# Performance work log

Hardware: AMD Instinct MI355X
Metric: run time of the kernel (lower is better)

Reference implementation:

```python
import jax, jax.numpy as jnp
import numpy as np

B, T, S, D, H, F = 4, 1024, 1024, 1024, 16, 4096
NEG = jnp.float32(-1e9)


def _ln(x, g, b):
    m = jnp.mean(x, axis=-1, keepdims=True)
    v = jnp.mean((x - m) ** 2, axis=-1, keepdims=True)
    return (x - m) * jax.lax.rsqrt(v + 1e-5) * g + b


def _mha(q, k, v, wq, bq, wk, bk, wv, bv, wo, bo, scale, mask, causal, sbias):
    Bq, Tq, Dq = q.shape
    Sk = k.shape[1]
    dk = Dq // H
    Q = (q @ wq.T + bq).reshape(Bq, Tq, H, dk).transpose(0, 2, 1, 3)  # [B,H,T,dk]
    K = (k @ wk.T + bk).reshape(Bq, Sk, H, dk).transpose(0, 2, 1, 3)  # [B,H,S,dk]
    V = (v @ wv.T + bv).reshape(Bq, Sk, H, dk).transpose(0, 2, 1, 3)
    s = jnp.einsum('bhtd,bhsd->bhts', Q, K) / jnp.sqrt(jnp.float32(dk))
    if sbias is not None:
        s = s + scale * sbias[:, None, None, :]
    if mask is not None:
        s = jnp.where(mask == 0, NEG, s)
    if causal is not None:
        s = jnp.where(causal == 0, NEG, s)
    a = jax.nn.softmax(s, axis=-1)
    o = jnp.einsum('bhts,bhsd->bhtd', a, V).transpose(0, 2, 1, 3).reshape(Bq, Tq, Dq)
    return o @ wo.T + bo


def setup_inputs():
    key = jax.random.key(0)
    ks = jax.random.split(key, 16)
    r = lambda i, shape, s=0.02: jax.random.normal(ks[i], shape, dtype=jnp.float32) * s
    z = lambda *shape: jnp.zeros(shape, jnp.float32)
    o = lambda *shape: jnp.ones(shape, jnp.float32)
    inp = dict(
        x=r(0, (B, T, D), 1.0),
        memory=r(1, (B, S, D), 1.0),
        sentence_bias=r(2, (B, S), 1.0),
        trg_mask=jnp.ones((B, 1, 1, T), jnp.int32),
        trg_causal_mask=jnp.tril(jnp.ones((T, T), jnp.int32))[None, None],
        src_mask=jnp.ones((B, 1, 1, S), jnp.int32),
        sa_wq=r(3, (D, D)), sa_bq=z(D), sa_wk=r(4, (D, D)), sa_bk=z(D),
        sa_wv=r(5, (D, D)), sa_bv=z(D), sa_wo=r(6, (D, D)), sa_bo=z(D),
        sa_scale=jnp.float32(0.1),
        ca_wq=r(7, (D, D)), ca_bq=z(D), ca_wk=r(8, (D, D)), ca_bk=z(D),
        ca_wv=r(9, (D, D)), ca_bv=z(D), ca_wo=r(10, (D, D)), ca_bo=z(D),
        ca_scale=jnp.float32(0.1),
        ln1_g=o(D), ln1_b=z(D), ln2_g=o(D), ln2_b=z(D), ln3_g=o(D), ln3_b=z(D),
        ffn_w1=r(11, (F, D)), ffn_b1=z(F), ffn_w2=r(12, (D, F)), ffn_b2=z(D),
    )
    return inp


def reference(x, memory, trg_mask, trg_causal_mask, src_mask, sentence_bias,
              sa_wq, sa_bq, sa_wk, sa_bk, sa_wv, sa_bv, sa_wo, sa_bo, sa_scale,
              ca_wq, ca_bq, ca_wk, ca_bk, ca_wv, ca_bv, ca_wo, ca_bo, ca_scale,
              ln1_g, ln1_b, ln2_g, ln2_b, ln3_g, ln3_b,
              ffn_w1, ffn_b1, ffn_w2, ffn_b2):
    # Faithful quirk: Q comes from normed x, K/V from raw residual stream.
    x = x + _mha(_ln(x, ln1_g, ln1_b), x, x,
                 sa_wq, sa_bq, sa_wk, sa_bk, sa_wv, sa_bv, sa_wo, sa_bo,
                 sa_scale, trg_mask, trg_causal_mask, None)
    x = x + _mha(_ln(x, ln2_g, ln2_b), memory, memory,
                 ca_wq, ca_bq, ca_wk, ca_bk, ca_wv, ca_bv, ca_wo, ca_bo,
                 ca_scale, src_mask, None, sentence_bias)
    h = _ln(x, ln3_g, ln3_b)
    x = x + (jax.nn.relu(h @ ffn_w1.T + ffn_b1) @ ffn_w2.T + ffn_b2)
    return x
```

## Files before the change

kernel.cpp:

```cpp
#include <hip/hip_runtime.h>
#include <hip/hip_bf16.h>
#include <cmath>
#include <stdint.h>

typedef __hip_bfloat16 bf16;
typedef __attribute__((ext_vector_type(8))) __bf16 bf16x8;
typedef __attribute__((ext_vector_type(8))) unsigned short u16x8;
typedef __attribute__((ext_vector_type(4))) float f32x4;

__device__ __forceinline__ void gld16(const void* g, const void* l)
{
    __builtin_amdgcn_global_load_lds(
        (const __attribute__((address_space(1))) unsigned int*)(unsigned long long)g,
        (__attribute__((address_space(3))) unsigned int*)(unsigned int)(unsigned long long)l,
        16, 0, 0);
}

struct CvtSrcs { const float* p[24]; };

__global__ __launch_bounds__(256) void cvt_all(CvtSrcs s, bf16* __restrict__ dst)
{
    const int i = (blockIdx.x * 256 + threadIdx.x) * 8;
    const int seg = i >> 20;
    const float* sp = s.p[seg] + (i & 1048575);
    const float4 a = *(const float4*)(sp);
    const float4 b = *(const float4*)(sp + 4);
    const float v[8] = {a.x, a.y, a.z, a.w, b.x, b.y, b.z, b.w};
    bf16 tmp[8];
#pragma unroll
    for (int j = 0; j < 8; ++j) tmp[j] = __float2bfloat16(v[j]);
    *(uint4*)(dst + i) = *(const uint4*)tmp;
}

enum {
    EPI_QSCALE = 0,
    EPI_KV = 1,
    EPI_RELU = 2,
    EPI_RES_F32_F32OUT = 3,
    EPI_PART = 4
};

template <int EPI>
__global__ __launch_bounds__(512, 2) void gemm256(
    const bf16* __restrict__ A, const bf16* __restrict__ W,
    const float* __restrict__ bias, void* __restrict__ out,
    int N, int Kiter, int Kstride)
{
    __shared__ __align__(16) unsigned short sA[2][2][128 * 64];
    __shared__ __align__(16) unsigned short sB[2][2][128 * 64];

    const int t  = threadIdx.x;
    const int l  = t & 63;
    const int w  = t >> 6;
    const int wv = w * 64;
    const int wr = w >> 2;
    const int wc = w & 3;
    const int lm = l & 15;
    const int kq = l >> 4;
    const int rx = lm & 7;

    int bx = blockIdx.x;
    if (EPI == EPI_PART) {
        const int chunk = bx >> 6;
        bx &= 63;
        A += (size_t)chunk * 1024;
        W += (size_t)chunk * 1024;
        out = (void*)((bf16*)out + (size_t)chunk * 4096 * 1024);
    }
    const int xcd = bx & 7;
    const int ib  = bx >> 3;
    const int bm  = xcd * 2 + (ib & 1);
    const int bn  = ib >> 1;

    const bf16* gA = A + (size_t)(bm * 256 + (t >> 3)) * Kstride
                       + ((t & 7) ^ ((t >> 3) & 7)) * 8;
    const bf16* gB = W + (size_t)(bn * 256 + (t >> 3)) * Kstride
                       + ((t & 7) ^ ((t >> 3) & 7)) * 8;

#define STAGE(slot, kt)                                                       \
    do {                                                                      \
        _Pragma("unroll")                                                     \
        for (int h = 0; h < 2; ++h) {                                         \
            _Pragma("unroll")                                                 \
            for (int j = 0; j < 2; ++j) {                                     \
                gld16(gA + (size_t)(h * 128 + j * 64) * Kstride + (kt) * 64,  \
                      &sA[slot][h][(j * 512 + wv) * 8]);                      \
                gld16(gB + (size_t)(h * 128 + j * 64) * Kstride + (kt) * 64,  \
                      &sB[slot][h][(j * 512 + wv) * 8]);                      \
            }                                                                 \
        }                                                                     \
    } while (0)

    STAGE(0, 0);
    __syncthreads();

    f32x4 acc[8][4] = {};
    const int NT = Kiter >> 6;

    for (int tt = 0; tt < NT; ++tt) {
        const int s = tt & 1;
        if (tt + 1 < NT) STAGE(s ^ 1, tt + 1);

#pragma unroll
        for (int q = 0; q < 4; ++q) {
            const int mh = q >> 1, nh = q & 1;
            bf16x8 af[4][2], bg[2][2];
#pragma unroll
            for (int mi = 0; mi < 4; ++mi)
#pragma unroll
                for (int kk = 0; kk < 2; ++kk) {
                    const int lr = mh * 64 + mi * 16 + lm;
                    const int sl = ((kk << 2) | kq) ^ rx;
                    af[mi][kk] = __builtin_bit_cast(bf16x8,
                        *(const u16x8*)(&sA[s][wr][lr * 64 + sl * 8]));
                }
#pragma unroll
            for (int ni = 0; ni < 2; ++ni)
#pragma unroll
                for (int kk = 0; kk < 2; ++kk) {
                    const int lr = (wc & 1) * 64 + nh * 32 + ni * 16 + lm;
                    const int sl = ((kk << 2) | kq) ^ rx;
                    bg[ni][kk] = __builtin_bit_cast(bf16x8,
                        *(const u16x8*)(&sB[s][wc >> 1][lr * 64 + sl * 8]));
                }
            __builtin_amdgcn_s_setprio(1);
#pragma unroll
            for (int mi = 0; mi < 4; ++mi)
#pragma unroll
                for (int ni = 0; ni < 2; ++ni)
#pragma unroll
                    for (int kk = 0; kk < 2; ++kk)
                        acc[mh * 4 + mi][nh * 2 + ni] =
                            __builtin_amdgcn_mfma_f32_16x16x32_bf16(
                                af[mi][kk], bg[ni][kk],
                                acc[mh * 4 + mi][nh * 2 + ni], 0, 0, 0);
            __builtin_amdgcn_s_setprio(0);
        }
        __syncthreads();
    }
#undef STAGE

#pragma unroll
    for (int NI = 0; NI < 4; ++NI) {
        const int col = bn * 256 + wc * 64 + NI * 16 + lm;
        const float bv = (EPI == EPI_PART) ? 0.f : bias[col];
#pragma unroll
        for (int MI = 0; MI < 8; ++MI) {
            const int row = bm * 256 + wr * 128 + MI * 16 + kq * 4;
#pragma unroll
            for (int r = 0; r < 4; ++r) {
                float v = acc[MI][NI][r] + bv;
                if (EPI == EPI_RELU) v = fmaxf(v, 0.f);
                ((bf16*)out)[(size_t)(row + r) * N + col] = __float2bfloat16(v);
            }
        }
    }
}

template <int EPI, int BM>
__global__ __launch_bounds__(BM * 2, 2) void gemm_bt(
    const bf16* __restrict__ A, const bf16* __restrict__ W,
    const float* __restrict__ bias, const float* __restrict__ bias2,
    const float* __restrict__ res, void* __restrict__ out,
    int M, int N, int Kiter, int Kstride)
{
    constexpr int T    = BM * 2;
    constexpr int ISSA = (BM * 4) / T;
    constexpr int ISSB = 512 / T;
    constexpr int ROWS = T / 4;
    constexpr int MBK  = 4096 / BM;
    constexpr int MBX  = MBK / 8;
    constexpr int MBS  = (BM == 64) ? 3 : 2;

    __shared__ __align__(16) unsigned short sA[2][BM * 32];
    __shared__ __align__(16) unsigned short sB[2][128 * 32];

    const int t  = threadIdx.x;
    const int l  = t & 63;
    const int w  = t >> 6;
    const int wv = w * 64;
    const int wm = (w >> 1) * 64;
    const int wn = (w & 1) * 64;
    const int lm = l & 15;
    const int kq = l >> 4;

    int bx = blockIdx.x;
    const int xcd = bx & 7;
    const int ib  = bx >> 3;
    const int bm  = xcd * MBX + (ib & (MBX - 1));
    const int bn  = ib >> MBS;

    const bf16* gA = A + (size_t)(bm * BM + (t >> 2)) * Kstride + (t & 3) * 8;
    const bf16* gB = W + (size_t)(bn * 128 + (t >> 2)) * Kstride + (t & 3) * 8;

    int aoffs[4], boffs[4];
#pragma unroll
    for (int i = 0; i < 4; ++i) {
        aoffs[i] = (wm + i * 16 + lm) * 32 + kq * 8;
        boffs[i] = (wn + i * 16 + lm) * 32 + kq * 8;
    }

#define STAGE(buf, kk)                                                       \
    do {                                                                     \
        _Pragma("unroll")                                                    \
        for (int j = 0; j < ISSA; ++j)                                       \
            gld16(gA + (size_t)j * ROWS * Kstride + (kk),                    \
                  &sA[buf][(j * T + wv) * 8]);                               \
        _Pragma("unroll")                                                    \
        for (int j = 0; j < ISSB; ++j)                                       \
            gld16(gB + (size_t)j * ROWS * Kstride + (kk),                    \
                  &sB[buf][(j * T + wv) * 8]);                               \
    } while (0)

    STAGE(0, 0);
    __syncthreads();

    f32x4 acc[4][4] = {};

    for (int k0 = 0; k0 < Kiter; k0 += 32) {
        const int cur = (k0 >> 5) & 1;

        if (k0 + 32 < Kiter) STAGE(cur ^ 1, k0 + 32);

        bf16x8 af[4], bg[4];
#pragma unroll
        for (int i = 0; i < 4; ++i)
            af[i] = __builtin_bit_cast(bf16x8, *(const u16x8*)(&sA[cur][aoffs[i]]));
#pragma unroll
        for (int i = 0; i < 4; ++i)
            bg[i] = __builtin_bit_cast(bf16x8, *(const u16x8*)(&sB[cur][boffs[i]]));
#pragma unroll
        for (int mi = 0; mi < 4; ++mi)
#pragma unroll
            for (int ni = 0; ni < 4; ++ni)
                acc[mi][ni] = __builtin_amdgcn_mfma_f32_16x16x32_bf16(
                    af[mi], bg[ni], acc[mi][ni], 0, 0, 0);

        __syncthreads();
    }
#undef STAGE

#pragma unroll
    for (int ni = 0; ni < 4; ++ni) {
        const int col = bn * 128 + wn + ni * 16 + lm;
        float bv = 0.f;
        if (EPI == EPI_KV) bv = (col < 1024) ? bias[col] : bias2[col - 1024];
        else bv = bias[col];
#pragma unroll
        for (int mi = 0; mi < 4; ++mi) {
#pragma unroll
            for (int r = 0; r < 4; ++r) {
                const int row = bm * BM + wm + mi * 16 + kq * 4 + r;
                float v = acc[mi][ni][r] + bv;
                if (EPI == EPI_QSCALE) v *= 0.125f;
                if (EPI == EPI_KV) {
                    if (col < 1024) {
                        ((bf16*)out)[(size_t)row * 1024 + col] = __float2bfloat16(v);
                    } else {
                        const int ch = col - 1024;
                        const size_t idx = (size_t)4 * 1048576 +
                            ((size_t)((row >> 10) * 16 + (ch >> 6)) * 64 + (ch & 63)) * 1024
                            + (row & 1023);
                        ((bf16*)out)[idx] = __float2bfloat16(v);
                    }
                } else if (EPI == EPI_RES_F32_F32OUT) {
                    const size_t idx = (size_t)row * N + col;
                    ((float*)out)[idx] = v + res[idx];
                } else {
                    ((bf16*)out)[(size_t)row * N + col] = __float2bfloat16(v);
                }
            }
        }
    }
}

__global__ __launch_bounds__(256) void ffn2_reduce(
    const bf16* __restrict__ P, const float* __restrict__ x2,
    const float* __restrict__ b2, float* __restrict__ out)
{
    const int i = (blockIdx.x * 256 + threadIdx.x) * 8;
    float v[8];
    {
        const float4 a = *(const float4*)(x2 + i);
        const float4 b = *(const float4*)(x2 + i + 4);
        v[0]=a.x; v[1]=a.y; v[2]=a.z; v[3]=a.w; v[4]=b.x; v[5]=b.y; v[6]=b.z; v[7]=b.w;
    }
    const int cb = i & 1023;
#pragma unroll
    for (int j = 0; j < 8; ++j) v[j] += b2[cb + j];
#pragma unroll
    for (int c = 0; c < 4; ++c) {
        const u16x8 u = *(const u16x8*)(P + (size_t)c * 4194304 + i);
        const bf16x8 pb = __builtin_bit_cast(bf16x8, u);
#pragma unroll
        for (int j = 0; j < 8; ++j) v[j] += (float)pb[j];
    }
    float4 o0 = {v[0], v[1], v[2], v[3]}, o1 = {v[4], v[5], v[6], v[7]};
    *(float4*)(out + i) = o0;
    *(float4*)(out + i + 4) = o1;
}

template <bool CAUSAL, bool SBIAS>
__global__ __launch_bounds__(256, 2) void flash_attn(
    const bf16* __restrict__ Q, const bf16* __restrict__ K,
    const bf16* __restrict__ Vt, bf16* __restrict__ O,
    const float* __restrict__ sbias, const float* __restrict__ scale_ptr)
{
    __shared__ __align__(16) unsigned short sK[2][64 * 64];
    __shared__ __align__(16) unsigned short sV[2][64 * 64];
    __shared__ __align__(16) unsigned short sP[4 * 32 * 72];

    const int t  = threadIdx.x;
    const int l  = t & 63;
    const int w  = t >> 6;
    const int wv = w * 64;
    const int lm = l & 15;
    const int kq = l >> 4;

    const int qb = blockIdx.x & 7;
    const int bh = blockIdx.x >> 3;
    const int h  = bh & 15;
    const int b  = bh >> 4;

    const int tb = qb * 128 + w * 32;
    const size_t qrow0 = (size_t)(b * 1024 + tb) * 1024 + h * 64;

    bf16x8 qf[2][2];
#pragma unroll
    for (int mi = 0; mi < 2; ++mi)
#pragma unroll
        for (int kk = 0; kk < 2; ++kk)
            qf[mi][kk] = __builtin_bit_cast(bf16x8,
                *(const u16x8*)(Q + qrow0 + (size_t)(mi * 16 + lm) * 1024 + kk * 32 + kq * 8));

    float cs = 0.f; const float* sb = nullptr;
    if (SBIAS) { cs = scale_ptr[0]; sb = sbias + b * 1024; }

    const bf16* gK = K  + (size_t)(b * 1024 + (t >> 2)) * 1024 + h * 64 + (t & 3) * 8;
    const bf16* gV = Vt + (size_t)((b * 16 + h) * 64 + (t >> 2)) * 1024 + (t & 3) * 8;
    __bf16* sPw = (__bf16*)sP + w * 32 * 72;

#define STAGE_KV(buf, s0r)                                              \
    do {                                                                \
        gld16(gK + (size_t)(s0r) * 1024,      &sK[buf][wv * 8]);        \
        gld16(gK + (size_t)(s0r) * 1024 + 32, &sK[buf][wv * 8 + 2048]); \
        gld16(gV + (s0r),                     &sV[buf][wv * 8]);        \
        gld16(gV + (s0r) + 32,                &sV[buf][wv * 8 + 2048]); \
    } while (0)

    const int niter = CAUSAL ? (2 * qb + 2) : 16;

    STAGE_KV(0, 0);
    __syncthreads();

    f32x4 acc_o[2][4] = {};
    f32x4 l_run[2] = {};

    for (int it = 0; it < niter; ++it) {
        const int s0 = it * 64;
        const int cur = it & 1;

        if (it + 1 < niter) STAGE_KV(cur ^ 1, s0 + 64);

        f32x4 accs[2][4] = {};
#pragma unroll
        for (int ni = 0; ni < 4; ++ni)
#pragma unroll
            for (int kk = 0; kk < 2; ++kk) {
                const bf16x8 kf = __builtin_bit_cast(bf16x8,
                    *(const u16x8*)(&sK[cur][kk * 2048 + (ni * 16 + lm) * 32 + kq * 8]));
#pragma unroll
                for (int mi = 0; mi < 2; ++mi)
                    accs[mi][ni] = __builtin_amdgcn_mfma_f32_16x16x32_bf16(
                        qf[mi][kk], kf, accs[mi][ni], 0, 0, 0);
            }

        if (SBIAS) {
#pragma unroll
            for (int ni = 0; ni < 4; ++ni) {
                const float sv = cs * sb[s0 + ni * 16 + lm];
#pragma unroll
                for (int mi = 0; mi < 2; ++mi)
#pragma unroll
                    for (int r = 0; r < 4; ++r) accs[mi][ni][r] += sv;
            }
        }
        if (CAUSAL && (s0 + 63 > tb)) {
#pragma unroll
            for (int ni = 0; ni < 4; ++ni) {
                const int s = s0 + ni * 16 + lm;
#pragma unroll
                for (int mi = 0; mi < 2; ++mi)
#pragma unroll
                    for (int r = 0; r < 4; ++r)
                        if (s > tb + mi * 16 + kq * 4 + r) accs[mi][ni][r] = -1e30f;
            }
        }

#pragma unroll
        for (int mi = 0; mi < 2; ++mi)
#pragma unroll
            for (int ni = 0; ni < 4; ++ni)
#pragma unroll
                for (int r = 0; r < 4; ++r) {
                    const float e = __expf(accs[mi][ni][r]);
                    l_run[mi][r] += e;
                    sPw[(mi * 16 + kq * 4 + r) * 72 + ni * 16 + lm] = (__bf16)e;
                }

#pragma unroll
        for (int kk = 0; kk < 2; ++kk) {
            bf16x8 pf[2];
#pragma unroll
            for (int mi = 0; mi < 2; ++mi)
                pf[mi] = __builtin_bit_cast(bf16x8,
                    *(const u16x8*)(sPw + (mi * 16 + lm) * 72 + kk * 32 + kq * 8));
#pragma unroll
            for (int di = 0; di < 4; ++di) {
                const bf16x8 vf = __builtin_bit_cast(bf16x8,
                    *(const u16x8*)(&sV[cur][kk * 2048 + (di * 16 + lm) * 32 + kq * 8]));
#pragma unroll
                for (int mi = 0; mi < 2; ++mi)
                    acc_o[mi][di] = __builtin_amdgcn_mfma_f32_16x16x32_bf16(
                        pf[mi], vf, acc_o[mi][di], 0, 0, 0);
            }
        }

        __syncthreads();
    }
#undef STAGE_KV

#pragma unroll
    for (int mi = 0; mi < 2; ++mi) {
        f32x4 lt = l_run[mi];
#pragma unroll
        for (int x = 1; x < 16; x <<= 1)
#pragma unroll
            for (int r = 0; r < 4; ++r) lt[r] += __shfl_xor(lt[r], x, 64);
#pragma unroll
        for (int r = 0; r < 4; ++r) lt[r] = 1.f / lt[r];
#pragma unroll
        for (int di = 0; di < 4; ++di)
#pragma unroll
            for (int r = 0; r < 4; ++r) {
                const size_t idx = (size_t)(b * 1024 + tb + mi * 16 + kq * 4 + r) * 1024
                                 + h * 64 + di * 16 + lm;
                O[idx] = __float2bfloat16(acc_o[mi][di][r] * lt[r]);
            }
    }
}

__global__ __launch_bounds__(256) void ln_kernel(
    const float* __restrict__ xin, const float* __restrict__ g,
    const float* __restrict__ bta, bf16* __restrict__ out)
{
    const int row = blockIdx.x;
    const int t = threadIdx.x;
    const size_t base = (size_t)row * 1024 + t * 4;

    const float4 f = *(const float4*)(xin + base);
    const float v[4] = {f.x, f.y, f.z, f.w};
    float s1 = v[0] + v[1] + v[2] + v[3];
    float s2 = v[0]*v[0] + v[1]*v[1] + v[2]*v[2] + v[3]*v[3];
#pragma unroll
    for (int off = 32; off > 0; off >>= 1) {
        s1 += __shfl_xor(s1, off, 64);
        s2 += __shfl_xor(s2, off, 64);
    }
    __shared__ float r1[4], r2[4];
    if ((t & 63) == 0) { r1[t >> 6] = s1; r2[t >> 6] = s2; }
    __syncthreads();
    s1 = r1[0] + r1[1] + r1[2] + r1[3];
    s2 = r2[0] + r2[1] + r2[2] + r2[3];
    const float mean = s1 * (1.f / 1024.f);
    const float var  = s2 * (1.f / 1024.f) - mean * mean;
    const float rstd = rsqrtf(var + 1e-5f);
#pragma unroll
    for (int j = 0; j < 4; ++j) {
        const int c = t * 4 + j;
        out[base + j] = __float2bfloat16((v[j] - mean) * rstd * g[c] + bta[c]);
    }
}

extern "C" void kernel_launch(void* const* d_in, const int* in_sizes, int n_in,
                              void* d_out, int out_size, void* d_ws, size_t ws_size,
                              hipStream_t stream)
{
    const float* x       = (const float*)d_in[0];
    const float* memory  = (const float*)d_in[1];
    const float* sbias   = (const float*)d_in[2];
    const float* sa_bq = (const float*)d_in[7];
    const float* sa_bk = (const float*)d_in[9];
    const float* sa_bv = (const float*)d_in[11];
    const float* sa_bo = (const float*)d_in[13];
    const float* ca_bq = (const float*)d_in[16];
    const float* ca_bk = (const float*)d_in[18];
    const float* ca_bv = (const float*)d_in[20];
    const float* ca_bo = (const float*)d_in[22];
    const float* ca_scale = (const float*)d_in[23];
    const float* ln1_g = (const float*)d_in[24]; const float* ln1_b = (const float*)d_in[25];
    const float* ln2_g = (const float*)d_in[26]; const float* ln2_b = (const float*)d_in[27];
    const float* ln3_g = (const float*)d_in[28]; const float* ln3_b = (const float*)d_in[29];
    const float* b1 = (const float*)d_in[31];
    const float* b2 = (const float*)d_in[33];

    char* ws = (char*)d_ws;
    const size_t MB = (size_t)1 << 20;
    float* x1    = (float*)(ws + 0 * MB);
    float* x2    = (float*)(ws + 16 * MB);
    bf16* lnbuf  = (bf16*)(ws + 32 * MB);
    bf16* Qb     = (bf16*)(ws + 40 * MB);
    bf16* Kb     = (bf16*)(ws + 48 * MB);
    bf16* Vtb    = (bf16*)(ws + 56 * MB);
    bf16* Ob     = (bf16*)(ws + 64 * MB);
    bf16* ffnmid = (bf16*)(ws + 40 * MB);
    bf16* wx     = (bf16*)(ws + 72 * MB);
    bf16* wmem   = (bf16*)(ws + 80 * MB);
    bf16* bw     = (bf16*)(ws + 88 * MB);
    bf16* b_sa_wq = bw + 0 * 1048576, *b_sa_wk = bw + 1 * 1048576;
    bf16* b_sa_wo = bw + 3 * 1048576;
    bf16* b_ca_wq = bw + 4 * 1048576, *b_ca_wk = bw + 5 * 1048576;
    bf16* b_ca_wo = bw + 7 * 1048576;
    bf16* b_w1   = (bf16*)(ws + 104 * MB);
    bf16* b_w2   = (bf16*)(ws + 112 * MB);
    bf16* part   = (bf16*)(ws + 72 * MB);

    const int M = 4096;
    dim3 blk256(256), blk128(128), blk512(512);
    const dim3 gQ(512);
    const dim3 gKV(512);
    const dim3 gFA(512);
    const dim3 g256(256);

    CvtSrcs cs;
    for (int c = 0; c < 4; ++c) {
        cs.p[c]      = x + (size_t)c * 1048576;
        cs.p[4 + c]  = memory + (size_t)c * 1048576;
        cs.p[16 + c] = (const float*)d_in[30] + (size_t)c * 1048576;
        cs.p[20 + c] = (const float*)d_in[32] + (size_t)c * 1048576;
    }
    cs.p[8]  = (const float*)d_in[6];
    cs.p[9]  = (const float*)d_in[8];
    cs.p[10] = (const float*)d_in[10];
    cs.p[11] = (const float*)d_in[12];
    cs.p[12] = (const float*)d_in[15];
    cs.p[13] = (const float*)d_in[17];
    cs.p[14] = (const float*)d_in[19];
    cs.p[15] = (const float*)d_in[21];
    cvt_all<<<24 * 1048576 / 2048, blk256, 0, stream>>>(cs, wx);

    ln_kernel<<<4096, blk256, 0, stream>>>(x, ln1_g, ln1_b, lnbuf);
    gemm_bt<EPI_QSCALE, 64><<<gQ, blk128, 0, stream>>>(
        lnbuf, b_sa_wq, sa_bq, nullptr, nullptr, Qb, M, 1024, 1024, 1024);
    gemm_bt<EPI_KV, 128><<<gKV, blk256, 0, stream>>>(
        wx, b_sa_wk, sa_bk, sa_bv, nullptr, Kb, M, 2048, 1024, 1024);
    flash_attn<true, false><<<gFA, blk256, 0, stream>>>(Qb, Kb, Vtb, Ob, nullptr, nullptr);
    gemm_bt<EPI_RES_F32_F32OUT, 64><<<gQ, blk128, 0, stream>>>(
        Ob, b_sa_wo, sa_bo, nullptr, x, x1, M, 1024, 1024, 1024);

    ln_kernel<<<4096, blk256, 0, stream>>>(x1, ln2_g, ln2_b, lnbuf);
    gemm_bt<EPI_QSCALE, 64><<<gQ, blk128, 0, stream>>>(
        lnbuf, b_ca_wq, ca_bq, nullptr, nullptr, Qb, M, 1024, 1024, 1024);
    gemm_bt<EPI_KV, 128><<<gKV, blk256, 0, stream>>>(
        wmem, b_ca_wk, ca_bk, ca_bv, nullptr, Kb, M, 2048, 1024, 1024);
    flash_attn<false, true><<<gFA, blk256, 0, stream>>>(Qb, Kb, Vtb, Ob, sbias, ca_scale);
    gemm_bt<EPI_RES_F32_F32OUT, 64><<<gQ, blk128, 0, stream>>>(
        Ob, b_ca_wo, ca_bo, nullptr, x1, x2, M, 1024, 1024, 1024);

    ln_kernel<<<4096, blk256, 0, stream>>>(x2, ln3_g, ln3_b, lnbuf);
    gemm256<EPI_RELU><<<g256, blk512, 0, stream>>>(
        lnbuf, b_w1, b1, ffnmid, 4096, 1024, 1024);
    gemm256<EPI_PART><<<g256, blk512, 0, stream>>>(
        ffnmid, b_w2, nullptr, part, 1024, 1024, 4096);
    ffn2_reduce<<<2048, blk256, 0, stream>>>(part, x2, b2, (float*)d_out);
}
```

Before: 505.3 us.

## Interleave split global-to-LDS loads with MFMA quadrants using vmcnt-gated barriers

```diff
diff --git a/kernel.cpp b/kernel.cpp
--- a/kernel.cpp
+++ b/kernel.cpp
@@ -77,68 +77,103 @@
     const bf16* gB = W + (size_t)(bn * 256 + (t >> 3)) * Kstride
                        + ((t & 7) ^ ((t >> 3) & 7)) * 8;
 
-#define STAGE(slot, kt)                                                       \
-    do {                                                                      \
-        _Pragma("unroll")                                                     \
-        for (int h = 0; h < 2; ++h) {                                         \
-            _Pragma("unroll")                                                 \
-            for (int j = 0; j < 2; ++j) {                                     \
-                gld16(gA + (size_t)(h * 128 + j * 64) * Kstride + (kt) * 64,  \
-                      &sA[slot][h][(j * 512 + wv) * 8]);                      \
-                gld16(gB + (size_t)(h * 128 + j * 64) * Kstride + (kt) * 64,  \
-                      &sB[slot][h][(j * 512 + wv) * 8]);                      \
-            }                                                                 \
-        }                                                                     \
+#define SQA(slot, kt, j)                                        \
+    gld16(gA + (size_t)((j) * 64) * Kstride + (kt) * 64,        \
+          &sA[slot][(j) >> 1][(((j) & 1) * 512 + wv) * 8])
+#define SQB(slot, kt, j)                                        \
+    gld16(gB + (size_t)((j) * 64) * Kstride + (kt) * 64,        \
+          &sB[slot][(j) >> 1][(((j) & 1) * 512 + wv) * 8])
+
+    bf16x8 af[4][2], bg[2][2];
+
+#define READ_AF(s_, mh)                                                     \
+    do {                                                                    \
+        _Pragma("unroll")                                                   \
+        for (int mi = 0; mi < 4; ++mi)                                      \
+            _Pragma("unroll")                                               \
+            for (int kk = 0; kk < 2; ++kk) {                                \
+                const int lr = (mh) * 64 + mi * 16 + lm;                    \
+                const int sl = ((kk << 2) | kq) ^ rx;                       \
+                af[mi][kk] = __builtin_bit_cast(bf16x8,                     \
+                    *(const u16x8*)(&sA[s_][wr][lr * 64 + sl * 8]));        \
+            }                                                               \
     } while (0)
-
-    STAGE(0, 0);
-    __syncthreads();
+#define READ_BG(s_, nh)                                                     \
+    do {                                                                    \
+        _Pragma("unroll")                                                   \
+        for (int ni = 0; ni < 2; ++ni)                                      \
+            _Pragma("unroll")                                               \
+            for (int kk = 0; kk < 2; ++kk) {                                \
+                const int lr = (wc & 1) * 64 + (nh) * 32 + ni * 16 + lm;    \
+                const int sl = ((kk << 2) | kq) ^ rx;                       \
+                bg[ni][kk] = __builtin_bit_cast(bf16x8,                     \
+                    *(const u16x8*)(&sB[s_][wc >> 1][lr * 64 + sl * 8]));   \
+            }                                                               \
+    } while (0)
+#define MFMA_QUAD(mh, nh)                                                   \
+    do {                                                                    \
+        __builtin_amdgcn_s_setprio(1);                                      \
+        _Pragma("unroll")                                                   \
+        for (int mi = 0; mi < 4; ++mi)                                      \
+            _Pragma("unroll")                                               \
+            for (int ni = 0; ni < 2; ++ni)                                  \
+                _Pragma("unroll")                                           \
+                for (int kk = 0; kk < 2; ++kk)                              \
+                    acc[(mh) * 4 + mi][(nh) * 2 + ni] =                     \
+                        __builtin_amdgcn_mfma_f32_16x16x32_bf16(            \
+                            af[mi][kk], bg[ni][kk],                         \
+                            acc[(mh) * 4 + mi][(nh) * 2 + ni], 0, 0, 0);    \
+        __builtin_amdgcn_s_setprio(0);                                      \
+    } while (0)
+#define BARRIER() do { __builtin_amdgcn_s_barrier();                        \
+                       __builtin_amdgcn_sched_barrier(0); } while (0)
+#define WAITV2() asm volatile("s_waitcnt vmcnt(2)" ::: "memory")
+#define WAITV0() asm volatile("s_waitcnt vmcnt(0)" ::: "memory")
 
     f32x4 acc[8][4] = {};
     const int NT = Kiter >> 6;
 
-    for (int tt = 0; tt < NT; ++tt) {
-        const int s = tt & 1;
-        if (tt + 1 < NT) STAGE(s ^ 1, tt + 1);
-
-#pragma unroll
-        for (int q = 0; q < 4; ++q) {
-            const int mh = q >> 1, nh = q & 1;
-            bf16x8 af[4][2], bg[2][2];
-#pragma unroll
-            for (int mi = 0; mi < 4; ++mi)
-#pragma unroll
-                for (int kk = 0; kk < 2; ++kk) {
-                    const int lr = mh * 64 + mi * 16 + lm;
-                    const int sl = ((kk << 2) | kq) ^ rx;
-                    af[mi][kk] = __builtin_bit_cast(bf16x8,
-                        *(const u16x8*)(&sA[s][wr][lr * 64 + sl * 8]));
-                }
-#pragma unroll
-            for (int ni = 0; ni < 2; ++ni)
-#pragma unroll
-                for (int kk = 0; kk < 2; ++kk) {
-                    const int lr = (wc & 1) * 64 + nh * 32 + ni * 16 + lm;
-                    const int sl = ((kk << 2) | kq) ^ rx;
-                    bg[ni][kk] = __builtin_bit_cast(bf16x8,
-                        *(const u16x8*)(&sB[s][wc >> 1][lr * 64 + sl * 8]));
-                }
-            __builtin_amdgcn_s_setprio(1);
-#pragma unroll
-            for (int mi = 0; mi < 4; ++mi)
-#pragma unroll
-                for (int ni = 0; ni < 2; ++ni)
-#pragma unroll
-                    for (int kk = 0; kk < 2; ++kk)
-                        acc[mh * 4 + mi][nh * 2 + ni] =
-                            __builtin_amdgcn_mfma_f32_16x16x32_bf16(
-                                af[mi][kk], bg[ni][kk],
-                                acc[mh * 4 + mi][nh * 2 + ni], 0, 0, 0);
-            __builtin_amdgcn_s_setprio(0);
-        }
-        __syncthreads();
-    }
-#undef STAGE
+    SQB(0, 0, 0); SQB(0, 0, 1); SQB(0, 0, 2); SQB(0, 0, 3);
+    SQA(0, 0, 0); SQA(0, 0, 2); SQA(0, 0, 1); SQA(0, 0, 3);
+
+    for (int tt = 0; tt < NT - 1; ++tt) {
+        const int s = tt & 1, d = s ^ 1, kn = tt + 1;
+        WAITV2(); BARRIER();
+        SQB(d, kn, 0); SQB(d, kn, 1);
+        READ_AF(s, 0); READ_BG(s, 0);
+        MFMA_QUAD(0, 0);
+        WAITV2(); BARRIER();
+        SQB(d, kn, 2); SQB(d, kn, 3);
+        READ_AF(s, 1);
+        MFMA_QUAD(1, 0);
+        SQA(d, kn, 0); SQA(d, kn, 2);
+        READ_BG(s, 1);
+        MFMA_QUAD(1, 1);
+        SQA(d, kn, 1); SQA(d, kn, 3);
+        READ_AF(s, 0);
+        MFMA_QUAD(0, 1);
+    }
+    {
+        const int s = (NT - 1) & 1;
+        WAITV2(); BARRIER();
+        READ_AF(s, 0); READ_BG(s, 0);
+        MFMA_QUAD(0, 0);
+        WAITV0(); BARRIER();
+        READ_AF(s, 1);
+        MFMA_QUAD(1, 0);
+        READ_BG(s, 1);
+        MFMA_QUAD(1, 1);
+        READ_AF(s, 0);
+        MFMA_QUAD(0, 1);
+    }
+#undef SQA
+#undef SQB
+#undef READ_AF
+#undef READ_BG
+#undef MFMA_QUAD
+#undef BARRIER
+#undef WAITV2
+#undef WAITV0
 
 #pragma unroll
     for (int NI = 0; NI < 4; ++NI) {
```

Measured after the change: 501.9 us. Within noise of the previous version (-0.7%).
